# Kernel tuning notes

Measured on AMD Instinct MI355X. Metric: run time of the kernel, lower is better.

Reference implementation:

```python
import jax, jax.numpy as jnp
import numpy as np

B = 32        # number of groups (batch.unique())
L = 512       # max_len (equal-size groups in this setup)
E = 512       # embed_dim
H = 8         # num_heads
N = B * L


def setup_inputs() -> dict:
    key = jax.random.key(0)
    k1, k2, k3 = jax.random.split(key, 3)
    embeddings = jax.random.normal(k1, (N, E), dtype=jnp.float32)
    # sorted group ids; equal group sizes keep max_len static for jit
    batch = jnp.repeat(jnp.arange(B, dtype=jnp.int32), L)
    in_proj_w = jax.random.normal(k2, (3 * E, E), dtype=jnp.float32) * (1.0 / np.sqrt(E))
    in_proj_b = jnp.zeros((3 * E,), dtype=jnp.float32)
    out_proj_w = jax.random.normal(k3, (E, E), dtype=jnp.float32) * (1.0 / np.sqrt(E))
    out_proj_b = jnp.zeros((E,), dtype=jnp.float32)
    return {"embeddings": embeddings, "batch": batch,
            "in_proj_w": in_proj_w, "in_proj_b": in_proj_b,
            "out_proj_w": out_proj_w, "out_proj_b": out_proj_b}


def reference(embeddings, batch, in_proj_w, in_proj_b, out_proj_w, out_proj_b):
    Dh = E // H
    ones = jnp.ones_like(batch, dtype=jnp.int32)
    counts = jax.ops.segment_sum(ones, batch, num_segments=B)          # [B]
    starts = jnp.cumsum(counts) - counts                               # exclusive cumsum
    pos = jnp.arange(N, dtype=jnp.int32) - starts[batch]               # position within group
    # pad ragged -> [B, L, E] (zeros for padding, as in torch code)
    padded = jnp.zeros((B, L, E), dtype=embeddings.dtype).at[batch, pos].set(embeddings)
    # FAITHFUL float attn_mask: +1.0 added to scores outside the valid block
    valid = (jnp.arange(L)[None, :] < counts[:, None]).astype(embeddings.dtype)  # [B, L]
    add_mask = 1.0 - valid[:, :, None] * valid[:, None, :]             # [B, Lq, Lk]

    qkv = padded @ in_proj_w.T + in_proj_b                             # [B, L, 3E]
    q, k, v = jnp.split(qkv, 3, axis=-1)
    q = q.reshape(B, L, H, Dh)
    k = k.reshape(B, L, H, Dh)
    v = v.reshape(B, L, H, Dh)
    scale = 1.0 / np.sqrt(Dh)
    scores = jnp.einsum('bqhd,bkhd->bhqk', q, k) * scale + add_mask[:, None, :, :]
    attn = jax.nn.softmax(scores, axis=-1)
    ctx = jnp.einsum('bhqk,bkhd->bqhd', attn, v).reshape(B, L, E)
    attn_out = ctx @ out_proj_w.T + out_proj_b                         # [B, L, E]
    # max_pool1d over sequence (includes padded query rows, as original)
    return jnp.max(attn_out, axis=1)                                   # [B, E]
```

## Files before the change

kernel.cpp:

```cpp
#include <hip/hip_runtime.h>
#include <math.h>


#define B_ 32
#define L_ 512
#define E_ 512
#define H_ 8
#define DH 64
#define N_ (B_ * L_)
#define EMB_N (N_ * E_)
#define IPW_N (3 * E_ * E_)
#define OPW_N (E_ * E_)

typedef _Float16 f16;
typedef __attribute__((ext_vector_type(8))) _Float16 f16x8;
typedef __attribute__((ext_vector_type(4))) float f32x4;
typedef unsigned short u16;

__device__ __forceinline__ u16 f16_bits(float x) {
    f16 h = (f16)x;
    return *reinterpret_cast<u16*>(&h);
}
__device__ __forceinline__ unsigned pk2(float a, float b) {
    return (unsigned)f16_bits(a) | ((unsigned)f16_bits(b) << 16);
}
__device__ __forceinline__ void async16(const void* g, void* l) {
    __builtin_amdgcn_global_load_lds(
        (const __attribute__((address_space(1))) void*)g,
        (__attribute__((address_space(3))) void*)l, 16, 0, 0);
}

__device__ __forceinline__ void atomicMaxFloat(float* addr, float val) {
    if (val >= 0.0f) atomicMax((int*)addr, __float_as_int(val));
    else             atomicMin((unsigned int*)addr, __float_as_uint(val));
}

__global__ __launch_bounds__(256) void cvt_kernel(
        const float* __restrict__ emb, const float* __restrict__ ipw,
        const float* __restrict__ opw,
        u16* __restrict__ eh, u16* __restrict__ wh, u16* __restrict__ oh,
        float* __restrict__ out) {
    if (blockIdx.x < 16) {
        int o = blockIdx.x * 1024 + threadIdx.x * 4;
        float4 ninf = make_float4(-INFINITY, -INFINITY, -INFINITY, -INFINITY);
        *(float4*)(out + o) = ninf;
    }
    size_t i = ((size_t)blockIdx.x * 256 + threadIdx.x) * 8;
    const float* src; u16* dst; size_t off;
    if (i < EMB_N)              { src = emb; dst = eh; off = i; }
    else if (i < EMB_N + IPW_N) { src = ipw; dst = wh; off = i - EMB_N; }
    else                        { src = opw; dst = oh; off = i - EMB_N - IPW_N; }
    float4 a = *(const float4*)(src + off);
    float4 b = *(const float4*)(src + off + 4);
    uint4 p;
    p.x = pk2(a.x, a.y); p.y = pk2(a.z, a.w);
    p.z = pk2(b.x, b.y); p.w = pk2(b.z, b.w);
    *(uint4*)(dst + off) = p;
}

__global__ __launch_bounds__(512) void qkv_mfma(
        const u16* __restrict__ Wg, const u16* __restrict__ Eg,
        const float* __restrict__ bias,
        u16* __restrict__ qg, u16* __restrict__ kg, u16* __restrict__ vg) {
    __shared__ u16 Ah[2][128 * 32];
    __shared__ u16 Bh[2][256 * 32];
    const int tok0 = blockIdx.x * 256, row0 = blockIdx.y * 128;
    const int tid = threadIdx.x, wave = tid >> 6, lane = tid & 63;
    const int quad = lane >> 4, c = lane & 15;
    const int ww = wave & 1, wt = wave >> 1;
    const int sw = (quad ^ ((c >> 1) & 3)) * 8;
    const bool vblk = (row0 >= 1024);

    f32x4 zero = {0.f, 0.f, 0.f, 0.f};
    f32x4 acc[4][4];
#pragma unroll
    for (int i = 0; i < 4; i++)
#pragma unroll
        for (int j = 0; j < 4; j++) acc[i][j] = zero;

    auto stage = [&](int buf, int kt) {
        {
            int chunk = wave * 64 + lane;
            int r = chunk >> 2, g = chunk & 3;
            int pos = g ^ ((r >> 1) & 3);
            async16(Wg + (size_t)(row0 + r) * E_ + kt * 32 + pos * 8,
                    &Ah[buf][wave * 512]);
        }
#pragma unroll
        for (int it = 0; it < 2; it++) {
            int chunk = (it * 8 + wave) * 64 + lane;
            int r = chunk >> 2, g = chunk & 3;
            int pos = g ^ ((r >> 1) & 3);
            async16(Eg + (size_t)(tok0 + r) * E_ + kt * 32 + pos * 8,
                    &Bh[buf][(it * 8 + wave) * 512]);
        }
    };

    stage(0, 0);
    for (int kt = 0; kt < 16; kt++) {
        __syncthreads();
        if (kt < 15) stage((kt + 1) & 1, kt + 1);
        const int buf = kt & 1;
        f16x8 mf[4], nf[4];
        if (!vblk) {
#pragma unroll
            for (int i = 0; i < 4; i++)
                mf[i] = *(const f16x8*)&Ah[buf][(ww * 64 + i * 16 + c) * 32 + sw];
#pragma unroll
            for (int j = 0; j < 4; j++)
                nf[j] = *(const f16x8*)&Bh[buf][(wt * 64 + j * 16 + c) * 32 + sw];
        } else {
#pragma unroll
            for (int i = 0; i < 4; i++)
                mf[i] = *(const f16x8*)&Bh[buf][(wt * 64 + i * 16 + c) * 32 + sw];
#pragma unroll
            for (int j = 0; j < 4; j++)
                nf[j] = *(const f16x8*)&Ah[buf][(ww * 64 + j * 16 + c) * 32 + sw];
        }
#pragma unroll
        for (int i = 0; i < 4; i++)
#pragma unroll
            for (int j = 0; j < 4; j++)
                acc[i][j] = __builtin_amdgcn_mfma_f32_16x16x32_f16(mf[i], nf[j], acc[i][j], 0, 0, 0);
    }

    if (!vblk) {
        const int which = row0 >> 9;
        u16* dst = which ? kg : qg;
        const float scale = which ? 1.0f : 0.18033688f;
        const int h = (((row0 & 511) + ww * 64) >> 6);
#pragma unroll
        for (int i = 0; i < 4; i++) {
            const int d0 = i * 16 + quad * 4;
            float4 bv = *(const float4*)(bias + row0 + ww * 64 + d0);
#pragma unroll
            for (int j = 0; j < 4; j++) {
                int n = tok0 + wt * 64 + j * 16 + c;
                int bb = n >> 9, l = n & 511;
                uint2 st;
                st.x = pk2((acc[i][j][0] + bv.x) * scale, (acc[i][j][1] + bv.y) * scale);
                st.y = pk2((acc[i][j][2] + bv.z) * scale, (acc[i][j][3] + bv.w) * scale);
                *(uint2*)(dst + (((size_t)(bb * H_ + h)) * L_ + l) * DH + d0) = st;
            }
        }
    } else {
        const int bb = tok0 >> 9;
        const int l0 = (tok0 & 511) + wt * 64;
#pragma unroll
        for (int j = 0; j < 4; j++) {
            int mw = row0 + ww * 64 + j * 16 + c;
            int h = (mw & 511) >> 6, d = mw & 63;
            float bv = bias[mw];
#pragma unroll
            for (int i = 0; i < 4; i++) {
                int l = l0 + i * 16 + quad * 4;
                uint2 st;
                st.x = pk2(acc[i][j][0] + bv, acc[i][j][1] + bv);
                st.y = pk2(acc[i][j][2] + bv, acc[i][j][3] + bv);
                *(uint2*)(vg + (((size_t)(bb * H_ + h)) * DH + d) * L_ + l) = st;
            }
        }
    }
}

__global__ __launch_bounds__(512) void attn_mfma(
        const u16* __restrict__ qg, const u16* __restrict__ kg,
        const u16* __restrict__ vg, u16* __restrict__ ctx) {
    __shared__ u16 ks[2][4096];
    __shared__ u16 vt[2][4096];
    __shared__ u16 ps[8][1024];
    const int qt = blockIdx.x, h = blockIdx.y, b = blockIdx.z;
    const int tid = threadIdx.x, wave = tid >> 6, lane = tid & 63;
    const int quad = lane >> 4, c = lane & 15;
    const size_t base = ((size_t)(b * H_ + h)) * (L_ * DH);

    f16x8 qf[2][2];
#pragma unroll
    for (int rs = 0; rs < 2; rs++)
#pragma unroll
        for (int kk = 0; kk < 2; kk++)
            qf[rs][kk] = *(const f16x8*)(qg + base +
                (size_t)(qt * 256 + wave * 32 + rs * 16 + c) * DH + kk * 32 + quad * 8);

    f32x4 zero = {0.f, 0.f, 0.f, 0.f};
    f32x4 Of[2][4];
    float lsum[2] = {0.f, 0.f};
#pragma unroll
    for (int rs = 0; rs < 2; rs++)
#pragma unroll
        for (int j = 0; j < 4; j++) Of[rs][j] = zero;

    auto stage = [&](int buf, int kt) {
        int chunk = wave * 64 + lane;
        int r = chunk >> 3, g = chunk & 7;
        int pos = g ^ (r & 7);
        async16(kg + base + (size_t)(kt * 64 + r) * DH + pos * 8, &ks[buf][wave * 512]);
        async16(vg + base + (size_t)r * L_ + kt * 64 + pos * 8, &vt[buf][wave * 512]);
    };

    stage(0, 0);
    for (int kt = 0; kt < 8; kt++) {
        __syncthreads();
        if (kt < 7) stage((kt + 1) & 1, kt + 1);
        const int buf = kt & 1;

        f16x8 kf[4][2];
#pragma unroll
        for (int jj = 0; jj < 4; jj++)
#pragma unroll
            for (int kk = 0; kk < 2; kk++)
                kf[jj][kk] = *(const f16x8*)&ks[buf][(jj * 16 + c) * 64 +
                                                    (((kk * 4 + quad) ^ (c & 7)) * 8)];
        f16x8 vf[2][4];
#pragma unroll
        for (int kk = 0; kk < 2; kk++)
#pragma unroll
            for (int j = 0; j < 4; j++)
                vf[kk][j] = *(const f16x8*)&vt[buf][(j * 16 + c) * 64 +
                                                    (((kk * 4 + quad) ^ (c & 7)) * 8)];

#pragma unroll
        for (int rs = 0; rs < 2; rs++) {
            f32x4 Sf[4];
#pragma unroll
            for (int jj = 0; jj < 4; jj++) {
                Sf[jj] = zero;
#pragma unroll
                for (int kk = 0; kk < 2; kk++)
                    Sf[jj] = __builtin_amdgcn_mfma_f32_16x16x32_f16(kf[jj][kk], qf[rs][kk], Sf[jj], 0, 0, 0);
            }
            unsigned pk[4][2];
            float rsum = 0.f;
#pragma unroll
            for (int jj = 0; jj < 4; jj++) {
                float p0 = exp2f(Sf[jj][0] - 6.0f), p1 = exp2f(Sf[jj][1] - 6.0f);
                float p2 = exp2f(Sf[jj][2] - 6.0f), p3 = exp2f(Sf[jj][3] - 6.0f);
                rsum += (p0 + p1) + (p2 + p3);
                pk[jj][0] = pk2(p0, p1);
                pk[jj][1] = pk2(p2, p3);
            }
            lsum[rs] += rsum;

            u16* psw = ps[wave];
#pragma unroll
            for (int jj = 0; jj < 4; jj++) {
                int addr = ((2 * jj + (quad >> 1)) * 16 + c) * 8 + 4 * (quad & 1);
                *(uint2*)&psw[addr] = make_uint2(pk[jj][0], pk[jj][1]);
            }
            f16x8 pf0 = *(const f16x8*)&psw[((0 * 4 + quad) * 16 + c) * 8];
            f16x8 pf1 = *(const f16x8*)&psw[((1 * 4 + quad) * 16 + c) * 8];
#pragma unroll
            for (int j = 0; j < 4; j++) {
                Of[rs][j] = __builtin_amdgcn_mfma_f32_16x16x32_f16(vf[0][j], pf0, Of[rs][j], 0, 0, 0);
                Of[rs][j] = __builtin_amdgcn_mfma_f32_16x16x32_f16(vf[1][j], pf1, Of[rs][j], 0, 0, 0);
            }
        }
    }

#pragma unroll
    for (int rs = 0; rs < 2; rs++) {
        float li = lsum[rs];
        li += __shfl_xor(li, 16);
        li += __shfl_xor(li, 32);
        float inv = 1.0f / li;
        int n = b * L_ + qt * 256 + wave * 32 + rs * 16 + c;
#pragma unroll
        for (int j = 0; j < 4; j++) {
            int d0 = j * 16 + quad * 4;
            uint2 st;
            st.x = pk2(Of[rs][j][0] * inv, Of[rs][j][1] * inv);
            st.y = pk2(Of[rs][j][2] * inv, Of[rs][j][3] * inv);
            *(uint2*)(ctx + (size_t)n * E_ + h * DH + d0) = st;
        }
    }
}

__global__ __launch_bounds__(256) void proj_mfma(
        const u16* __restrict__ Ag, const u16* __restrict__ Bg,
        const float* __restrict__ bias, float* __restrict__ out) {
    __shared__ u16 Ah[2][128 * 32], Bh[2][128 * 32];
    __shared__ float red[2][128];
    const int row0 = blockIdx.x * 128, col0 = blockIdx.y * 128;
    const int tid = threadIdx.x, wave = tid >> 6, lane = tid & 63;
    const int quad = lane >> 4, c = lane & 15;
    const int wr = (wave >> 1) * 64, wc = (wave & 1) * 64;
    const int sw = (quad ^ ((c >> 1) & 3)) * 8;

    f32x4 zero = {0.f, 0.f, 0.f, 0.f};
    f32x4 acc[4][4];
#pragma unroll
    for (int i = 0; i < 4; i++)
#pragma unroll
        for (int j = 0; j < 4; j++) acc[i][j] = zero;

    auto stage = [&](int buf, int kt) {
#pragma unroll
        for (int it = 0; it < 2; it++) {
            int chunk = (wave * 2 + it) * 64 + lane;
            int r = chunk >> 2, g = chunk & 3;
            int pos = g ^ ((r >> 1) & 3);
            int lbase = (wave * 2 + it) * 512;
            async16(Ag + (size_t)(row0 + r) * E_ + kt * 32 + pos * 8, &Ah[buf][lbase]);
            async16(Bg + (size_t)(col0 + r) * E_ + kt * 32 + pos * 8, &Bh[buf][lbase]);
        }
    };

    stage(0, 0);
    for (int kt = 0; kt < 16; kt++) {
        __syncthreads();
        if (kt < 15) stage((kt + 1) & 1, kt + 1);
        const int buf = kt & 1;
        f16x8 af[4], bf[4];
#pragma unroll
        for (int i = 0; i < 4; i++)
            af[i] = *(const f16x8*)&Ah[buf][(wr + i * 16 + c) * 32 + sw];
#pragma unroll
        for (int j = 0; j < 4; j++)
            bf[j] = *(const f16x8*)&Bh[buf][(wc + j * 16 + c) * 32 + sw];
#pragma unroll
        for (int i = 0; i < 4; i++)
#pragma unroll
            for (int j = 0; j < 4; j++)
                acc[i][j] = __builtin_amdgcn_mfma_f32_16x16x32_f16(af[i], bf[j], acc[i][j], 0, 0, 0);
    }

    float cm[4];
#pragma unroll
    for (int j = 0; j < 4; j++) {
        cm[j] = -INFINITY;
#pragma unroll
        for (int i = 0; i < 4; i++)
#pragma unroll
            for (int r = 0; r < 4; r++) cm[j] = fmaxf(cm[j], acc[i][j][r]);
        cm[j] = fmaxf(cm[j], __shfl_xor(cm[j], 16));
        cm[j] = fmaxf(cm[j], __shfl_xor(cm[j], 32));
    }
    if (quad == 0)
#pragma unroll
        for (int j = 0; j < 4; j++) red[wave >> 1][wc + j * 16 + c] = cm[j];
    __syncthreads();
    if (tid < 128) {
        int bb = row0 >> 9;
        float m = fmaxf(red[0][tid], red[1][tid]) + bias[col0 + tid];
        atomicMaxFloat(&out[(size_t)bb * E_ + col0 + tid], m);
    }
}

extern "C" void kernel_launch(void* const* d_in, const int* in_sizes, int n_in,
                              void* d_out, int out_size, void* d_ws, size_t ws_size,
                              hipStream_t stream) {
    const float* emb = (const float*)d_in[0];
    const float* ipw = (const float*)d_in[2];
    const float* ipb = (const float*)d_in[3];
    const float* opw = (const float*)d_in[4];
    const float* opb = (const float*)d_in[5];
    float* out = (float*)d_out;

    u16* eh  = (u16*)d_ws;
    u16* wh  = eh + EMB_N;
    u16* oh  = wh + IPW_N;
    u16* qg  = oh + OPW_N;
    u16* kg  = qg + (size_t)N_ * E_;
    u16* vg  = kg + (size_t)N_ * E_;
    u16* ctx = vg + (size_t)N_ * E_;

    cvt_kernel<<<(EMB_N + IPW_N + OPW_N) / (256 * 8), 256, 0, stream>>>(
        emb, ipw, opw, eh, wh, oh, out);
    qkv_mfma<<<dim3(N_ / 256, (3 * E_) / 128), 512, 0, stream>>>(
        wh, eh, ipb, qg, kg, vg);
    attn_mfma<<<dim3(L_ / 256, H_, B_), 512, 0, stream>>>(qg, kg, vg, ctx);
    proj_mfma<<<dim3(N_ / 128, E_ / 128), 256, 0, stream>>>(ctx, oh, opb, out);
}
```

Before: 167.8 us.

## Rebalance attention and output-projection work per wave and per block

```diff
diff --git a/kernel.cpp b/kernel.cpp
--- a/kernel.cpp
+++ b/kernel.cpp
@@ -163,39 +163,43 @@
     }
 }
 
-__global__ __launch_bounds__(512) void attn_mfma(
+__global__ __launch_bounds__(256) void attn_mfma(
         const u16* __restrict__ qg, const u16* __restrict__ kg,
         const u16* __restrict__ vg, u16* __restrict__ ctx) {
     __shared__ u16 ks[2][4096];
     __shared__ u16 vt[2][4096];
-    __shared__ u16 ps[8][1024];
+    __shared__ u16 ps[4][1024];
     const int qt = blockIdx.x, h = blockIdx.y, b = blockIdx.z;
     const int tid = threadIdx.x, wave = tid >> 6, lane = tid & 63;
     const int quad = lane >> 4, c = lane & 15;
     const size_t base = ((size_t)(b * H_ + h)) * (L_ * DH);
 
-    f16x8 qf[2][2];
-#pragma unroll
-    for (int rs = 0; rs < 2; rs++)
+    f16x8 qf[4][2];
+#pragma unroll
+    for (int rs = 0; rs < 4; rs++)
 #pragma unroll
         for (int kk = 0; kk < 2; kk++)
             qf[rs][kk] = *(const f16x8*)(qg + base +
-                (size_t)(qt * 256 + wave * 32 + rs * 16 + c) * DH + kk * 32 + quad * 8);
+                (size_t)(qt * 256 + wave * 64 + rs * 16 + c) * DH + kk * 32 + quad * 8);
 
     f32x4 zero = {0.f, 0.f, 0.f, 0.f};
-    f32x4 Of[2][4];
-    float lsum[2] = {0.f, 0.f};
-#pragma unroll
-    for (int rs = 0; rs < 2; rs++)
+    f32x4 Of[4][4];
+    float lsum[4] = {0.f, 0.f, 0.f, 0.f};
+#pragma unroll
+    for (int rs = 0; rs < 4; rs++)
 #pragma unroll
         for (int j = 0; j < 4; j++) Of[rs][j] = zero;
 
     auto stage = [&](int buf, int kt) {
-        int chunk = wave * 64 + lane;
-        int r = chunk >> 3, g = chunk & 7;
-        int pos = g ^ (r & 7);
-        async16(kg + base + (size_t)(kt * 64 + r) * DH + pos * 8, &ks[buf][wave * 512]);
-        async16(vg + base + (size_t)r * L_ + kt * 64 + pos * 8, &vt[buf][wave * 512]);
+#pragma unroll
+        for (int it = 0; it < 2; it++) {
+            int chunk = (wave * 2 + it) * 64 + lane;
+            int r = chunk >> 3, g = chunk & 7;
+            int pos = g ^ (r & 7);
+            int lbase = (wave * 2 + it) * 512;
+            async16(kg + base + (size_t)(kt * 64 + r) * DH + pos * 8, &ks[buf][lbase]);
+            async16(vg + base + (size_t)r * L_ + kt * 64 + pos * 8, &vt[buf][lbase]);
+        }
     };
 
     stage(0, 0);
@@ -220,7 +224,7 @@
                                                     (((kk * 4 + quad) ^ (c & 7)) * 8)];
 
 #pragma unroll
-        for (int rs = 0; rs < 2; rs++) {
+        for (int rs = 0; rs < 4; rs++) {
             f32x4 Sf[4];
 #pragma unroll
             for (int jj = 0; jj < 4; jj++) {
@@ -258,12 +262,12 @@
     }
 
 #pragma unroll
-    for (int rs = 0; rs < 2; rs++) {
+    for (int rs = 0; rs < 4; rs++) {
         float li = lsum[rs];
         li += __shfl_xor(li, 16);
         li += __shfl_xor(li, 32);
         float inv = 1.0f / li;
-        int n = b * L_ + qt * 256 + wave * 32 + rs * 16 + c;
+        int n = b * L_ + qt * 256 + wave * 64 + rs * 16 + c;
 #pragma unroll
         for (int j = 0; j < 4; j++) {
             int d0 = j * 16 + quad * 4;
@@ -275,15 +279,16 @@
     }
 }
 
-__global__ __launch_bounds__(256) void proj_mfma(
+__global__ __launch_bounds__(512) void proj_mfma(
         const u16* __restrict__ Ag, const u16* __restrict__ Bg,
         const float* __restrict__ bias, float* __restrict__ out) {
-    __shared__ u16 Ah[2][128 * 32], Bh[2][128 * 32];
-    __shared__ float red[2][128];
-    const int row0 = blockIdx.x * 128, col0 = blockIdx.y * 128;
+    __shared__ u16 Ah[2][256 * 32];
+    __shared__ u16 Bh[2][128 * 32];
+    __shared__ float red[4][128];
+    const int row0 = blockIdx.x * 256, col0 = blockIdx.y * 128;
     const int tid = threadIdx.x, wave = tid >> 6, lane = tid & 63;
     const int quad = lane >> 4, c = lane & 15;
-    const int wr = (wave >> 1) * 64, wc = (wave & 1) * 64;
+    const int ww = wave & 1, wt = wave >> 1;
     const int sw = (quad ^ ((c >> 1) & 3)) * 8;
 
     f32x4 zero = {0.f, 0.f, 0.f, 0.f};
@@ -296,12 +301,18 @@
     auto stage = [&](int buf, int kt) {
 #pragma unroll
         for (int it = 0; it < 2; it++) {
-            int chunk = (wave * 2 + it) * 64 + lane;
+            int chunk = (it * 8 + wave) * 64 + lane;
             int r = chunk >> 2, g = chunk & 3;
             int pos = g ^ ((r >> 1) & 3);
-            int lbase = (wave * 2 + it) * 512;
-            async16(Ag + (size_t)(row0 + r) * E_ + kt * 32 + pos * 8, &Ah[buf][lbase]);
-            async16(Bg + (size_t)(col0 + r) * E_ + kt * 32 + pos * 8, &Bh[buf][lbase]);
+            async16(Ag + (size_t)(row0 + r) * E_ + kt * 32 + pos * 8,
+                    &Ah[buf][(it * 8 + wave) * 512]);
+        }
+        {
+            int chunk = wave * 64 + lane;
+            int r = chunk >> 2, g = chunk & 3;
+            int pos = g ^ ((r >> 1) & 3);
+            async16(Bg + (size_t)(col0 + r) * E_ + kt * 32 + pos * 8,
+                    &Bh[buf][wave * 512]);
         }
     };
 
@@ -313,10 +324,10 @@
         f16x8 af[4], bf[4];
 #pragma unroll
         for (int i = 0; i < 4; i++)
-            af[i] = *(const f16x8*)&Ah[buf][(wr + i * 16 + c) * 32 + sw];
+            af[i] = *(const f16x8*)&Ah[buf][(wt * 64 + i * 16 + c) * 32 + sw];
 #pragma unroll
         for (int j = 0; j < 4; j++)
-            bf[j] = *(const f16x8*)&Bh[buf][(wc + j * 16 + c) * 32 + sw];
+            bf[j] = *(const f16x8*)&Bh[buf][(ww * 64 + j * 16 + c) * 32 + sw];
 #pragma unroll
         for (int i = 0; i < 4; i++)
 #pragma unroll
@@ -337,11 +348,12 @@
     }
     if (quad == 0)
 #pragma unroll
-        for (int j = 0; j < 4; j++) red[wave >> 1][wc + j * 16 + c] = cm[j];
+        for (int j = 0; j < 4; j++) red[wt][ww * 64 + j * 16 + c] = cm[j];
     __syncthreads();
     if (tid < 128) {
         int bb = row0 >> 9;
-        float m = fmaxf(red[0][tid], red[1][tid]) + bias[col0 + tid];
+        float m = fmaxf(fmaxf(red[0][tid], red[1][tid]),
+                        fmaxf(red[2][tid], red[3][tid])) + bias[col0 + tid];
         atomicMaxFloat(&out[(size_t)bb * E_ + col0 + tid], m);
     }
 }
@@ -368,6 +380,6 @@
         emb, ipw, opw, eh, wh, oh, out);
     qkv_mfma<<<dim3(N_ / 256, (3 * E_) / 128), 512, 0, stream>>>(
         wh, eh, ipb, qg, kg, vg);
-    attn_mfma<<<dim3(L_ / 256, H_, B_), 512, 0, stream>>>(qg, kg, vg, ctx);
-    proj_mfma<<<dim3(N_ / 128, E_ / 128), 256, 0, stream>>>(ctx, oh, opb, out);
-}
+    attn_mfma<<<dim3(L_ / 256, H_, B_), 256, 0, stream>>>(qg, kg, vg, ctx);
+    proj_mfma<<<dim3(N_ / 256, E_ / 128), 512, 0, stream>>>(ctx, oh, opb, out);
+}
```

Result: slower. 180.0 us (+7.2%).

## Store Q/K/V in MFMA-fragment order and load attention operands directly from global

Applied to the files above, without the earlier changes.

```diff
diff --git a/kernel.cpp b/kernel.cpp
--- a/kernel.cpp
+++ b/kernel.cpp
@@ -133,6 +133,7 @@
         for (int i = 0; i < 4; i++) {
             const int d0 = i * 16 + quad * 4;
             float4 bv = *(const float4*)(bias + row0 + ww * 64 + d0);
+            const int dch = i * 2 + (quad >> 1);
 #pragma unroll
             for (int j = 0; j < 4; j++) {
                 int n = tok0 + wt * 64 + j * 16 + c;
@@ -140,47 +141,53 @@
                 uint2 st;
                 st.x = pk2((acc[i][j][0] + bv.x) * scale, (acc[i][j][1] + bv.y) * scale);
                 st.y = pk2((acc[i][j][2] + bv.z) * scale, (acc[i][j][3] + bv.w) * scale);
-                *(uint2*)(dst + (((size_t)(bb * H_ + h)) * L_ + l) * DH + d0) = st;
+                size_t addr = (size_t)(bb * H_ + h) * 32768 +
+                              (l >> 4) * 1024 + dch * 128 + (l & 15) * 8 + (quad & 1) * 4;
+                *(uint2*)(dst + addr) = st;
             }
         }
     } else {
         const int bb = tok0 >> 9;
         const int l0 = (tok0 & 511) + wt * 64;
+        const int tt = l0 >> 6;
+        const int h = (((row0 & 511) + ww * 64) >> 6);
 #pragma unroll
         for (int j = 0; j < 4; j++) {
             int mw = row0 + ww * 64 + j * 16 + c;
-            int h = (mw & 511) >> 6, d = mw & 63;
+            int d = mw & 63;
             float bv = bias[mw];
 #pragma unroll
             for (int i = 0; i < 4; i++) {
-                int l = l0 + i * 16 + quad * 4;
                 uint2 st;
                 st.x = pk2(acc[i][j][0] + bv, acc[i][j][1] + bv);
                 st.y = pk2(acc[i][j][2] + bv, acc[i][j][3] + bv);
-                *(uint2*)(vg + (((size_t)(bb * H_ + h)) * DH + d) * L_ + l) = st;
-            }
-        }
-    }
-}
-
-__global__ __launch_bounds__(512) void attn_mfma(
+                size_t addr = (size_t)(bb * H_ + h) * 32768 + tt * 4096 +
+                              j * 1024 + (i * 2 + (quad >> 1)) * 128 +
+                              c * 8 + (quad & 1) * 4;
+                *(uint2*)(vg + addr) = st;
+            }
+        }
+    }
+}
+
+__global__ __launch_bounds__(256) void attn_mfma(
         const u16* __restrict__ qg, const u16* __restrict__ kg,
         const u16* __restrict__ vg, u16* __restrict__ ctx) {
-    __shared__ u16 ks[2][4096];
-    __shared__ u16 vt[2][4096];
-    __shared__ u16 ps[8][1024];
+    __shared__ u16 ps[4][1024];
     const int qt = blockIdx.x, h = blockIdx.y, b = blockIdx.z;
     const int tid = threadIdx.x, wave = tid >> 6, lane = tid & 63;
     const int quad = lane >> 4, c = lane & 15;
-    const size_t base = ((size_t)(b * H_ + h)) * (L_ * DH);
+    const size_t base = (size_t)(b * H_ + h) * 32768;
+    const int lane8 = lane * 8;
 
     f16x8 qf[2][2];
 #pragma unroll
-    for (int rs = 0; rs < 2; rs++)
+    for (int rs = 0; rs < 2; rs++) {
+        const size_t qb = base + (size_t)(qt * 8 + wave * 2 + rs) * 1024;
 #pragma unroll
         for (int kk = 0; kk < 2; kk++)
-            qf[rs][kk] = *(const f16x8*)(qg + base +
-                (size_t)(qt * 256 + wave * 32 + rs * 16 + c) * DH + kk * 32 + quad * 8);
+            qf[rs][kk] = *(const f16x8*)(qg + qb + kk * 512 + lane8);
+    }
 
     f32x4 zero = {0.f, 0.f, 0.f, 0.f};
     f32x4 Of[2][4];
@@ -190,34 +197,20 @@
 #pragma unroll
         for (int j = 0; j < 4; j++) Of[rs][j] = zero;
 
-    auto stage = [&](int buf, int kt) {
-        int chunk = wave * 64 + lane;
-        int r = chunk >> 3, g = chunk & 7;
-        int pos = g ^ (r & 7);
-        async16(kg + base + (size_t)(kt * 64 + r) * DH + pos * 8, &ks[buf][wave * 512]);
-        async16(vg + base + (size_t)r * L_ + kt * 64 + pos * 8, &vt[buf][wave * 512]);
-    };
-
-    stage(0, 0);
     for (int kt = 0; kt < 8; kt++) {
-        __syncthreads();
-        if (kt < 7) stage((kt + 1) & 1, kt + 1);
-        const int buf = kt & 1;
-
+        const size_t tb = base + (size_t)kt * 4096;
         f16x8 kf[4][2];
 #pragma unroll
         for (int jj = 0; jj < 4; jj++)
 #pragma unroll
             for (int kk = 0; kk < 2; kk++)
-                kf[jj][kk] = *(const f16x8*)&ks[buf][(jj * 16 + c) * 64 +
-                                                    (((kk * 4 + quad) ^ (c & 7)) * 8)];
+                kf[jj][kk] = *(const f16x8*)(kg + tb + jj * 1024 + kk * 512 + lane8);
         f16x8 vf[2][4];
 #pragma unroll
         for (int kk = 0; kk < 2; kk++)
 #pragma unroll
             for (int j = 0; j < 4; j++)
-                vf[kk][j] = *(const f16x8*)&vt[buf][(j * 16 + c) * 64 +
-                                                    (((kk * 4 + quad) ^ (c & 7)) * 8)];
+                vf[kk][j] = *(const f16x8*)(vg + tb + j * 1024 + kk * 512 + lane8);
 
 #pragma unroll
         for (int rs = 0; rs < 2; rs++) {
@@ -263,7 +256,7 @@
         li += __shfl_xor(li, 16);
         li += __shfl_xor(li, 32);
         float inv = 1.0f / li;
-        int n = b * L_ + qt * 256 + wave * 32 + rs * 16 + c;
+        int n = b * L_ + qt * 128 + wave * 32 + rs * 16 + c;
 #pragma unroll
         for (int j = 0; j < 4; j++) {
             int d0 = j * 16 + quad * 4;
@@ -368,6 +361,6 @@
         emb, ipw, opw, eh, wh, oh, out);
     qkv_mfma<<<dim3(N_ / 256, (3 * E_) / 128), 512, 0, stream>>>(
         wh, eh, ipb, qg, kg, vg);
-    attn_mfma<<<dim3(L_ / 256, H_, B_), 512, 0, stream>>>(qg, kg, vg, ctx);
+    attn_mfma<<<dim3(L_ / 128, H_, B_), 256, 0, stream>>>(qg, kg, vg, ctx);
     proj_mfma<<<dim3(N_ / 128, E_ / 128), 256, 0, stream>>>(ctx, oh, opb, out);
 }
```

New measurement: 167.3 us. No clear change (-0.3%).
